# Kernel optimization log

Measured on AMD Instinct MI355X. Metric: run time of the kernel, lower is better.

The kernel has to match this reference:

```python
import jax, jax.numpy as jnp
import numpy as np

B, S, D = 2, 2048, 1024   # batch, seq, d_model
L, H = 256, 512           # d_latent, d_hidden (expert MLP)
E = 8                     # num_experts
SH = 512                  # shared-expert hidden (= d_hidden)


def setup_inputs() -> dict:
    key = jax.random.key(0)
    ks = jax.random.split(key, 12)
    s = 0.02
    return {
        "x": jax.random.normal(ks[0], (B, S, D), dtype=jnp.float32),
        "w_router": jax.random.normal(ks[1], (E, D), dtype=jnp.float32) * s,
        "w_down": jax.random.normal(ks[2], (L, D), dtype=jnp.float32) * s,
        "w_up": jax.random.normal(ks[3], (D, L), dtype=jnp.float32) * s,
        "w1_e": jax.random.normal(ks[4], (E, H, L), dtype=jnp.float32) * s,
        "wg_e": jax.random.normal(ks[5], (E, H, L), dtype=jnp.float32) * s,
        "w2_e": jax.random.normal(ks[6], (E, L, H), dtype=jnp.float32) * s,
        "w1_s": jax.random.normal(ks[7], (SH, D), dtype=jnp.float32) * s,
        "wg_s": jax.random.normal(ks[8], (SH, D), dtype=jnp.float32) * s,
        "w2_s": jax.random.normal(ks[9], (D, SH), dtype=jnp.float32) * s,
        "top_k": 2,
    }


def reference(x, w_router, w_down, w_up, w1_e, wg_e, w2_e, w1_s, wg_s, w2_s, top_k):
    Bq, Sq, Dq = x.shape
    T = Bq * Sq
    xf = x.reshape(T, Dq)

    # --- router (fp32 logits, softmax over top-k values) ---
    logits = xf.astype(jnp.float32) @ w_router.T            # (T, E)
    topk_val, topk_idx = jax.lax.top_k(logits, top_k)       # (T, k)
    topk_w = jax.nn.softmax(topk_val, axis=-1).astype(x.dtype)
    # dense combine weights (T, E); zero for unselected experts
    comb = jnp.zeros((T, E), dtype=x.dtype)
    comb = comb.at[jnp.arange(T)[:, None], topk_idx].add(topk_w)

    # --- shared latent down-projection ---
    lat = xf @ w_down.T                                     # (T, L)

    # --- all-expert SwiGLU in latent space, then weighted combine ---
    g = jax.nn.silu(jnp.einsum('tl,ehl->teh', lat, wg_e))   # (T, E, H)
    a = jnp.einsum('tl,ehl->teh', lat, w1_e)                # (T, E, H)
    ex = jnp.einsum('teh,elh->tel', g * a, w2_e)            # (T, E, L)
    routed_lat = jnp.einsum('te,tel->tl', comb, ex)         # (T, L)
    routed = routed_lat @ w_up.T                            # (T, D)

    # --- shared (dense) SwiGLU expert in d_model ---
    shared = (jax.nn.silu(xf @ wg_s.T) * (xf @ w1_s.T)) @ w2_s.T

    y = routed + shared
    return y.reshape(Bq, Sq, Dq)
```

## Files before the change

kernel.cpp:

```cpp
#include <hip/hip_runtime.h>
#include <hip/hip_bf16.h>
#include <math.h>

#define T_TOK 4096
#define D_MODEL 1024
#define L_LAT 256
#define H_HID 512
#define E_EXP 8
#define SH_HID 512
#define TOT_EROWS (2 * T_TOK)

typedef __bf16 bf16x8 __attribute__((ext_vector_type(8)));
typedef float f32x4 __attribute__((ext_vector_type(4)));

__device__ __forceinline__ unsigned short f2bf(float f) {
    union { float f; unsigned int u; } c{f};
    unsigned int r = (c.u + 0x7fffu + ((c.u >> 16) & 1u)) >> 16;
    return (unsigned short)r;
}
__device__ __forceinline__ float bf2f(unsigned short u) {
    union { unsigned int u; float f; } c{(unsigned int)u << 16};
    return c.f;
}

__device__ __forceinline__ void gload_lds16(const unsigned short* g, unsigned short* l) {
    __builtin_amdgcn_global_load_lds(
        (const __attribute__((address_space(1))) void*)g,
        (__attribute__((address_space(3))) void*)l,
        16, 0, 0);
}

__device__ __forceinline__ int swz64(int row, int s) {
    return s ^ (row & 7);
}

__global__ __launch_bounds__(256)
void cast_router_kernel(const float* __restrict__ x, const float* __restrict__ w_router,
                        const float* __restrict__ w_down, const float* __restrict__ wg_s,
                        const float* __restrict__ w1_s,
                        unsigned short* __restrict__ xb, unsigned short* __restrict__ wdb,
                        unsigned short* __restrict__ wgsb, unsigned short* __restrict__ w1sb,
                        int* __restrict__ topk_idx, float* __restrict__ topk_w)
{
    __shared__ float wlds[E_EXP * D_MODEL];
    int bid = blockIdx.x;
    int tid = threadIdx.x;

    if (bid < 4096) {
        int j = (bid * 256 + tid) * 4;
        float4 v = *(const float4*)(x + j);
        ushort4 o = { f2bf(v.x), f2bf(v.y), f2bf(v.z), f2bf(v.w) };
        *(ushort4*)(xb + j) = o;
        return;
    }
    if (bid >= 5120) {
        int i = (bid - 5120) * 256 + tid;
        const float* src; unsigned short* dst; int base;
        if      (i < 65536)  { src = w_down; dst = wdb;  base = 0; }
        else if (i < 196608) { src = wg_s;   dst = wgsb; base = 65536; }
        else                 { src = w1_s;   dst = w1sb; base = 196608; }
        int j = (i - base) * 4;
        float4 v = *(const float4*)(src + j);
        ushort4 o = { f2bf(v.x), f2bf(v.y), f2bf(v.z), f2bf(v.w) };
        *(ushort4*)(dst + j) = o;
        return;
    }

    int rb = bid - 4096;
    for (int i = tid * 4; i < E_EXP * D_MODEL; i += 256 * 4)
        *(float4*)(wlds + i) = *(const float4*)(w_router + i);
    __syncthreads();

    int wid = tid >> 6, lane = tid & 63;
    int t = rb * 4 + wid;
    const float* xr = x + (size_t)t * D_MODEL;
    float acc[E_EXP];
#pragma unroll
    for (int e = 0; e < E_EXP; ++e) acc[e] = 0.f;
#pragma unroll 4
    for (int i = 0; i < D_MODEL / 64; ++i) {
        int d = lane + i * 64;
        float xv = xr[d];
#pragma unroll
        for (int e = 0; e < E_EXP; ++e)
            acc[e] = fmaf(xv, wlds[e * D_MODEL + d], acc[e]);
    }
#pragma unroll
    for (int e = 0; e < E_EXP; ++e)
        for (int off = 32; off > 0; off >>= 1)
            acc[e] += __shfl_xor(acc[e], off, 64);
    if (lane == 0) {
        int i0 = 0; float v0 = acc[0];
#pragma unroll
        for (int e = 1; e < E_EXP; ++e) if (acc[e] > v0) { v0 = acc[e]; i0 = e; }
        int i1 = -1; float v1 = -INFINITY;
#pragma unroll
        for (int e = 0; e < E_EXP; ++e) if (e != i0 && acc[e] > v1) { v1 = acc[e]; i1 = e; }
        float e1 = expf(v1 - v0);
        topk_idx[2 * t] = i0; topk_idx[2 * t + 1] = i1;
        topk_w[2 * t] = 1.f / (1.f + e1);
        topk_w[2 * t + 1] = e1 / (1.f + e1);
    }
}

__device__ void bucket_body(const int* __restrict__ topk_idx,
                            int* __restrict__ counts, int* __restrict__ offsets,
                            int* __restrict__ tok_of_row, int* __restrict__ row_of_pair,
                            int* sb)
{
    int* s_wavecnt  = sb;
    int* s_wavebase = sb + 32;
    int* s_tot      = sb + 64;
    int* s_off      = sb + 72;
    int tid = threadIdx.x, wave = tid >> 6, lane = tid & 63;
    int base_i = tid * 32;

    int cnt[E_EXP];
#pragma unroll
    for (int e = 0; e < E_EXP; ++e) cnt[e] = 0;
#pragma unroll
    for (int j = 0; j < 32; ++j) {
        int e = topk_idx[base_i + j];
#pragma unroll
        for (int q = 0; q < E_EXP; ++q) cnt[q] += (e == q) ? 1 : 0;
    }
    int excl[E_EXP];
#pragma unroll
    for (int e = 0; e < E_EXP; ++e) {
        int v = cnt[e];
#pragma unroll
        for (int off = 1; off < 64; off <<= 1) {
            int u = __shfl_up(v, off, 64);
            v += (lane >= off) ? u : 0;
        }
        excl[e] = v - cnt[e];
        if (lane == 63) s_wavecnt[wave * 8 + e] = v;
    }
    __syncthreads();
    if (tid < E_EXP) {
        int tot = 0;
        for (int w = 0; w < 4; ++w) tot += s_wavecnt[w * 8 + tid];
        s_tot[tid] = tot;
        counts[tid] = tot;
    }
    __syncthreads();
    if (tid == 0) {
        int off = 0;
        for (int e = 0; e < E_EXP; ++e) { s_off[e] = off; offsets[e] = off; off += s_tot[e]; }
    }
    __syncthreads();
    if (tid < E_EXP) {
        int run = s_off[tid];
        for (int w = 0; w < 4; ++w) { s_wavebase[w * 8 + tid] = run; run += s_wavecnt[w * 8 + tid]; }
    }
    __syncthreads();
    int tb[E_EXP];
#pragma unroll
    for (int e = 0; e < E_EXP; ++e) tb[e] = s_wavebase[wave * 8 + e] + excl[e];
#pragma unroll
    for (int j = 0; j < 32; ++j) {
        int item = base_i + j;
        int e = topk_idx[item];
        int p = 0;
#pragma unroll
        for (int q = 0; q < E_EXP; ++q) if (e == q) { p = tb[q]; tb[q] = p + 1; }
        tok_of_row[p] = item >> 1;
        row_of_pair[item] = p;
    }
}

template<bool DUAL, bool SILU, bool EXPERT, bool GATHER, int OUT_MODE>
__device__ void gemm_tile(unsigned short* As, unsigned short* Bs0, unsigned short* Bs1,
                          int m0, int n0, int e,
                          const unsigned short* __restrict__ A,
                          const unsigned short* __restrict__ B0g,
                          const unsigned short* __restrict__ B1g,
                          void* __restrict__ Cv,
                          int M, int K, int ldc,
                          const int* __restrict__ tok_of_row,
                          const int* __restrict__ offsets,
                          const int* __restrict__ counts,
                          long strideB)
{
    int m_base = EXPERT ? offsets[e] : 0;
    int m_count = EXPERT ? counts[e] : M;
    if (m0 >= m_count) return;

    const unsigned short* B0 = B0g + (EXPERT ? (size_t)e * strideB : 0);
    const unsigned short* B1 = DUAL ? (B1g + (EXPERT ? (size_t)e * strideB : 0)) : nullptr;

    int tid = threadIdx.x;
    int r8 = tid >> 3, slot = tid & 7;

    const unsigned short* aptr[4];
#pragma unroll
    for (int r = 0; r < 4; ++r) {
        int rl = r * 32 + r8;
        int mrow = m0 + rl;
        if (mrow >= m_count) mrow = m_count - 1;
        long grow;
        if (GATHER)      grow = tok_of_row[m_base + mrow];
        else if (EXPERT) grow = m_base + mrow;
        else             grow = mrow;
        aptr[r] = A + (size_t)grow * K + swz64(rl, slot) * 8;
    }
    const unsigned short* bptr0[2];
    const unsigned short* bptr1[2];
#pragma unroll
    for (int r = 0; r < 2; ++r) {
        int rl = r * 32 + r8;
        int gs = swz64(rl, slot) * 8;
        bptr0[r] = B0 + (size_t)(n0 + rl) * K + gs;
        if (DUAL) bptr1[r] = B1 + (size_t)(n0 + rl) * K + gs;
    }
    unsigned short* As_dst  = As  + tid * 8;
    unsigned short* Bs0_dst = Bs0 + tid * 8;
    unsigned short* Bs1_dst = DUAL ? (Bs1 + tid * 8) : nullptr;

    int wave = tid >> 6, lane = tid & 63;
    int wm0 = (wave >> 1) * 64, wn0 = (wave & 1) * 32;
    int l15 = lane & 15, kg = lane >> 4;

    f32x4 acc0[4][2] = {};
    f32x4 acc1[DUAL ? 4 : 1][DUAL ? 2 : 1] = {};

    for (int k0 = 0; k0 < K; k0 += 64) {
#pragma unroll
        for (int r = 0; r < 4; ++r)
            gload_lds16(aptr[r] + k0, As_dst + r * 2048);
#pragma unroll
        for (int r = 0; r < 2; ++r) {
            gload_lds16(bptr0[r] + k0, Bs0_dst + r * 2048);
            if constexpr (DUAL) gload_lds16(bptr1[r] + k0, Bs1_dst + r * 2048);
        }
        __syncthreads();

        bf16x8 af[2][4];
#pragma unroll
        for (int kh = 0; kh < 2; ++kh)
#pragma unroll
            for (int mf = 0; mf < 4; ++mf) {
                int row = wm0 + mf * 16 + l15;
                af[kh][mf] = *reinterpret_cast<const bf16x8*>(As + row * 64 + swz64(row, kh * 4 + kg) * 8);
            }
        bf16x8 bf0[2][2], bf1[2][2];
#pragma unroll
        for (int kh = 0; kh < 2; ++kh)
#pragma unroll
            for (int nf = 0; nf < 2; ++nf) {
                int row = wn0 + nf * 16 + l15;
                bf0[kh][nf] = *reinterpret_cast<const bf16x8*>(Bs0 + row * 64 + swz64(row, kh * 4 + kg) * 8);
                if constexpr (DUAL)
                    bf1[kh][nf] = *reinterpret_cast<const bf16x8*>(Bs1 + row * 64 + swz64(row, kh * 4 + kg) * 8);
            }
#pragma unroll
        for (int kh = 0; kh < 2; ++kh)
#pragma unroll
            for (int mf = 0; mf < 4; ++mf)
#pragma unroll
                for (int nf = 0; nf < 2; ++nf) {
                    acc0[mf][nf] = __builtin_amdgcn_mfma_f32_16x16x32_bf16(af[kh][mf], bf0[kh][nf], acc0[mf][nf], 0, 0, 0);
                    if constexpr (DUAL)
                        acc1[mf][nf] = __builtin_amdgcn_mfma_f32_16x16x32_bf16(af[kh][mf], bf1[kh][nf], acc1[mf][nf], 0, 0, 0);
                }
        __syncthreads();
    }

#pragma unroll
    for (int mf = 0; mf < 4; ++mf) {
#pragma unroll
        for (int r4 = 0; r4 < 4; ++r4) {
            int mrow = m0 + wm0 + mf * 16 + kg * 4 + r4;
            if (mrow >= m_count) continue;
            size_t crow = (size_t)((EXPERT ? m_base : 0) + mrow) * ldc + n0 + wn0;
#pragma unroll
            for (int nf = 0; nf < 2; ++nf) {
                float v = acc0[mf][nf][r4];
                if constexpr (SILU) {
                    float g = v;
                    float a = acc1[mf][nf][r4];
                    v = (g / (1.f + expf(-g))) * a;
                }
                int col = nf * 16 + l15;
                if constexpr (OUT_MODE == 1)      ((unsigned short*)Cv)[crow + col] = f2bf(v);
                else if constexpr (OUT_MODE == 2) ((float*)Cv)[crow + col] += v;
                else                              ((float*)Cv)[crow + col] = v;
            }
        }
    }
}

__global__ __launch_bounds__(256)
void k_main(const unsigned short* __restrict__ x_bf,
            const unsigned short* __restrict__ wdown_bf,
            const unsigned short* __restrict__ wgs_bf,
            const unsigned short* __restrict__ w1s_bf,
            const float* __restrict__ wg_e, const float* __restrict__ w1_e,
            const float* __restrict__ w2_e,
            const float* __restrict__ w_up, const float* __restrict__ w2_s,
            unsigned short* __restrict__ lat_bf,
            unsigned short* __restrict__ hs,
            unsigned short* __restrict__ wge_bf, unsigned short* __restrict__ w1e_bf,
            unsigned short* __restrict__ w2e_bf, unsigned short* __restrict__ wup_bf,
            unsigned short* __restrict__ w2s_bf,
            const int* __restrict__ topk_idx,
            int* __restrict__ counts, int* __restrict__ offsets,
            int* __restrict__ tok_of_row, int* __restrict__ row_of_pair)
{
    __shared__ __align__(16) unsigned short As[128 * 64];
    __shared__ __align__(16) unsigned short Bs0[64 * 64];
    __shared__ __align__(16) unsigned short Bs1[64 * 64];

    int bid = blockIdx.x;
    int tid = threadIdx.x;

    if (bid == 384) {
        bucket_body(topk_idx, counts, offsets, tok_of_row, row_of_pair, (int*)As);
        return;
    }
    if (bid > 384) {
        int i = (bid - 385) * 256 + tid;
        const float* src; unsigned short* dst; int base;
        if      (i < 262144) { src = wg_e; dst = wge_bf; base = 0; }
        else if (i < 524288) { src = w1_e; dst = w1e_bf; base = 262144; }
        else if (i < 786432) { src = w2_e; dst = w2e_bf; base = 524288; }
        else if (i < 851968) { src = w_up; dst = wup_bf; base = 786432; }
        else                 { src = w2_s; dst = w2s_bf; base = 851968; }
        int j = (i - base) * 4;
        float4 v = *(const float4*)(src + j);
        ushort4 o = { f2bf(v.x), f2bf(v.y), f2bf(v.z), f2bf(v.w) };
        *(ushort4*)(dst + j) = o;
        return;
    }

    int xq = bid & 31, y = bid >> 5;
    if (y < 4) {
        gemm_tile<false, false, false, false, 1>(As, Bs0, Bs1, xq * 128, y * 64, 0,
            x_bf, wdown_bf, nullptr, lat_bf, T_TOK, D_MODEL, L_LAT,
            nullptr, nullptr, nullptr, 0);
    } else {
        gemm_tile<true, true, false, false, 1>(As, Bs0, Bs1, xq * 128, (y - 4) * 64, 0,
            x_bf, wgs_bf, w1s_bf, hs, T_TOK, D_MODEL, SH_HID,
            nullptr, nullptr, nullptr, 0);
    }
}

__global__ __launch_bounds__(256)
void k_exp_sh(const unsigned short* __restrict__ lat_bf,
              const unsigned short* __restrict__ wge_bf,
              const unsigned short* __restrict__ w1e_bf,
              const unsigned short* __restrict__ hs,
              const unsigned short* __restrict__ w2s_bf,
              unsigned short* __restrict__ hbuf_bf,
              float* __restrict__ out,
              const int* __restrict__ tok_of_row,
              const int* __restrict__ offsets,
              const int* __restrict__ counts)
{
    __shared__ __align__(16) unsigned short As[128 * 64];
    __shared__ __align__(16) unsigned short Bs0[64 * 64];
    __shared__ __align__(16) unsigned short Bs1[64 * 64];

    int bid = blockIdx.x;
    if (bid < 4096) {
        int xq = bid >> 6, e = (bid >> 3) & 7, y = bid & 7;
        gemm_tile<true, true, true, true, 1>(As, Bs0, Bs1, xq * 128, y * 64, e,
            lat_bf, wge_bf, w1e_bf, hbuf_bf, 0, L_LAT, H_HID,
            tok_of_row, offsets, counts, (long)H_HID * L_LAT);
    } else {
        int idx = bid - 4096;
        int xq = idx & 31, y = idx >> 5;
        gemm_tile<false, false, false, false, 0>(As, Bs0, Bs1, xq * 128, y * 64, 0,
            hs, w2s_bf, nullptr, out, T_TOK, SH_HID, D_MODEL,
            nullptr, nullptr, nullptr, 0);
    }
}

__global__ __launch_bounds__(256)
void k_expdown(const unsigned short* __restrict__ hbuf_bf,
               const unsigned short* __restrict__ w2e_bf,
               unsigned short* __restrict__ ex_bf,
               const int* __restrict__ offsets,
               const int* __restrict__ counts)
{
    __shared__ __align__(16) unsigned short As[128 * 64];
    __shared__ __align__(16) unsigned short Bs0[64 * 64];
    __shared__ __align__(16) unsigned short Bs1[8];
    gemm_tile<false, false, true, false, 1>(As, Bs0, Bs1,
        blockIdx.x * 128, blockIdx.y * 64, blockIdx.z,
        hbuf_bf, w2e_bf, nullptr, ex_bf, 0, H_HID, L_LAT,
        nullptr, offsets, counts, (long)L_LAT * H_HID);
}

__global__ void combine_kernel(const unsigned short* __restrict__ ex,
                               const int* __restrict__ row_of_pair,
                               const float* __restrict__ topk_w,
                               unsigned short* __restrict__ rlat)
{
    int i = blockIdx.x * 256 + threadIdx.x;
    int t = i >> 6;
    int l4 = (i & 63) * 4;
    int r0 = row_of_pair[2 * t], r1 = row_of_pair[2 * t + 1];
    float w0 = topk_w[2 * t], w1 = topk_w[2 * t + 1];
    ushort4 a = *(const ushort4*)(ex + (size_t)r0 * L_LAT + l4);
    ushort4 b = *(const ushort4*)(ex + (size_t)r1 * L_LAT + l4);
    ushort4 o = { f2bf(w0 * bf2f(a.x) + w1 * bf2f(b.x)),
                  f2bf(w0 * bf2f(a.y) + w1 * bf2f(b.y)),
                  f2bf(w0 * bf2f(a.z) + w1 * bf2f(b.z)),
                  f2bf(w0 * bf2f(a.w) + w1 * bf2f(b.w)) };
    *(ushort4*)(rlat + (size_t)t * L_LAT + l4) = o;
}

__global__ __launch_bounds__(256)
void k_final(const unsigned short* __restrict__ rlat,
             const unsigned short* __restrict__ wup_bf,
             float* __restrict__ out)
{
    __shared__ __align__(16) unsigned short As[128 * 64];
    __shared__ __align__(16) unsigned short Bs0[64 * 64];
    __shared__ __align__(16) unsigned short Bs1[8];
    gemm_tile<false, false, false, false, 2>(As, Bs0, Bs1,
        blockIdx.x * 128, blockIdx.y * 64, 0,
        rlat, wup_bf, nullptr, out, T_TOK, L_LAT, D_MODEL,
        nullptr, nullptr, nullptr, 0);
}

extern "C" void kernel_launch(void* const* d_in, const int* in_sizes, int n_in,
                              void* d_out, int out_size, void* d_ws, size_t ws_size,
                              hipStream_t stream)
{
    const float* x        = (const float*)d_in[0];
    const float* w_router = (const float*)d_in[1];
    const float* w_down   = (const float*)d_in[2];
    const float* w_up     = (const float*)d_in[3];
    const float* w1_e     = (const float*)d_in[4];
    const float* wg_e     = (const float*)d_in[5];
    const float* w2_e     = (const float*)d_in[6];
    const float* w1_s     = (const float*)d_in[7];
    const float* wg_s     = (const float*)d_in[8];
    const float* w2_s     = (const float*)d_in[9];
    float* out = (float*)d_out;

    char* ws = (char*)d_ws;
    size_t off = 0;
    auto alloc = [&](size_t bytes) -> void* {
        void* p = ws + off;
        off += (bytes + 255) & ~(size_t)255;
        return p;
    };
    unsigned short* x_bf    = (unsigned short*)alloc((size_t)T_TOK * D_MODEL * 2);
    unsigned short* lat_bf  = (unsigned short*)alloc((size_t)T_TOK * L_LAT * 2);
    unsigned short* hs      = (unsigned short*)alloc((size_t)T_TOK * SH_HID * 2);
    unsigned short* rlat    = (unsigned short*)alloc((size_t)T_TOK * L_LAT * 2);
    unsigned short* ex_bf   = (unsigned short*)alloc((size_t)TOT_EROWS * L_LAT * 2);
    unsigned short* wdown_bf= (unsigned short*)alloc((size_t)L_LAT * D_MODEL * 2);
    unsigned short* wge_bf  = (unsigned short*)alloc((size_t)E_EXP * H_HID * L_LAT * 2);
    unsigned short* w1e_bf  = (unsigned short*)alloc((size_t)E_EXP * H_HID * L_LAT * 2);
    unsigned short* w2e_bf  = (unsigned short*)alloc((size_t)E_EXP * L_LAT * H_HID * 2);
    unsigned short* wgs_bf  = (unsigned short*)alloc((size_t)SH_HID * D_MODEL * 2);
    unsigned short* w1s_bf  = (unsigned short*)alloc((size_t)SH_HID * D_MODEL * 2);
    unsigned short* wup_bf  = (unsigned short*)alloc((size_t)D_MODEL * L_LAT * 2);
    unsigned short* w2s_bf  = (unsigned short*)alloc((size_t)D_MODEL * SH_HID * 2);
    int*   topk_idx    = (int*)alloc(T_TOK * 2 * 4);
    float* topk_w      = (float*)alloc(T_TOK * 2 * 4);
    int*   tok_of_row  = (int*)alloc(T_TOK * 2 * 4);
    int*   row_of_pair = (int*)alloc(T_TOK * 2 * 4);
    int*   counts      = (int*)alloc(E_EXP * 4);
    int*   offsets     = (int*)alloc(E_EXP * 4);
    unsigned short* hbuf_bf = x_bf;

    cast_router_kernel<<<6400, 256, 0, stream>>>(
        x, w_router, w_down, wg_s, w1_s,
        x_bf, wdown_bf, wgs_bf, w1s_bf, topk_idx, topk_w);

    k_main<<<4225, 256, 0, stream>>>(
        x_bf, wdown_bf, wgs_bf, w1s_bf, wg_e, w1_e, w2_e, w_up, w2_s,
        lat_bf, hs, wge_bf, w1e_bf, w2e_bf, wup_bf, w2s_bf,
        topk_idx, counts, offsets, tok_of_row, row_of_pair);

    k_exp_sh<<<4608, 256, 0, stream>>>(
        lat_bf, wge_bf, w1e_bf, hs, w2s_bf, hbuf_bf, out,
        tok_of_row, offsets, counts);

    k_expdown<<<dim3(TOT_EROWS / 128, L_LAT / 64, E_EXP), 256, 0, stream>>>(
        hbuf_bf, w2e_bf, ex_bf, offsets, counts);

    combine_kernel<<<T_TOK * L_LAT / 4 / 256, 256, 0, stream>>>(
        ex_bf, row_of_pair, topk_w, rlat);

    k_final<<<dim3(T_TOK / 128, D_MODEL / 64), 256, 0, stream>>>(rlat, wup_bf, out);
}
```

Before: 91.10 us.

## Fuse top-k combine into up-projection GEMM and widen tiles to 128x128

Adds a 128x128-tile GEMM variant. It is used for the shared down-projection, the expert down-projection and the final up-projection. The final GEMM now gathers the two expert rows per token and blends them with the top-k weights while loading the A tile, so the separate combine kernel and its rlat buffer are no longer needed. The blend path uses plain vector loads rather than direct global-to-LDS loads, and the larger tiles halve the block counts, which could reduce occupancy or load balance.

```diff
diff --git a/kernel.cpp b/kernel.cpp
--- a/kernel.cpp
+++ b/kernel.cpp
@@ -281,6 +281,140 @@
                     float a = acc1[mf][nf][r4];
                     v = (g / (1.f + expf(-g))) * a;
                 }
+                int col = nf * 16 + l15;
+                if constexpr (OUT_MODE == 1) ((unsigned short*)Cv)[crow + col] = f2bf(v);
+                else                         ((float*)Cv)[crow + col] = v;
+            }
+        }
+    }
+}
+
+template<bool EXPERT, int OUT_MODE, bool BLEND>
+__device__ void gemm_tile_n128(unsigned short* SM,
+                               int m0, int n0, int e,
+                               const unsigned short* __restrict__ A,
+                               const unsigned short* __restrict__ B0g,
+                               void* __restrict__ Cv,
+                               int M, int K, int ldc,
+                               const int* __restrict__ offsets,
+                               const int* __restrict__ counts,
+                               long strideB,
+                               const int* __restrict__ row_of_pair,
+                               const float* __restrict__ topk_w)
+{
+    unsigned short* As = SM;
+    unsigned short* Bs = SM + 128 * 64;
+
+    int m_base = EXPERT ? offsets[e] : 0;
+    int m_count = EXPERT ? counts[e] : M;
+    if (m0 >= m_count) return;
+
+    const unsigned short* B0 = B0g + (EXPERT ? (size_t)e * strideB : 0);
+
+    int tid = threadIdx.x;
+    int r8 = tid >> 3, slot = tid & 7;
+
+    const unsigned short* aptr[4];
+    const unsigned short* a2ptr[4];
+    float wa[4], wb[4];
+#pragma unroll
+    for (int r = 0; r < 4; ++r) {
+        int rl = r * 32 + r8;
+        int mrow = m0 + rl;
+        if (mrow >= m_count) mrow = m_count - 1;
+        if constexpr (BLEND) {
+            int t = m0 + rl;
+            int rp0 = row_of_pair[2 * t], rp1 = row_of_pair[2 * t + 1];
+            wa[r] = topk_w[2 * t]; wb[r] = topk_w[2 * t + 1];
+            aptr[r]  = A + (size_t)rp0 * K + swz64(rl, slot) * 8;
+            a2ptr[r] = A + (size_t)rp1 * K + swz64(rl, slot) * 8;
+        } else {
+            long grow = EXPERT ? (long)(m_base + mrow) : (long)mrow;
+            aptr[r] = A + (size_t)grow * K + swz64(rl, slot) * 8;
+        }
+    }
+    const unsigned short* bptr[4];
+#pragma unroll
+    for (int r = 0; r < 4; ++r) {
+        int rl = r * 32 + r8;
+        bptr[r] = B0 + (size_t)(n0 + rl) * K + swz64(rl, slot) * 8;
+    }
+    unsigned short* As_dst = As + tid * 8;
+    unsigned short* Bs_dst = Bs + tid * 8;
+
+    int wave = tid >> 6, lane = tid & 63;
+    int wm0 = (wave >> 1) * 64, wn0 = (wave & 1) * 64;
+    int l15 = lane & 15, kg = lane >> 4;
+
+    f32x4 acc[4][4] = {};
+
+    for (int k0 = 0; k0 < K; k0 += 64) {
+        if constexpr (BLEND) {
+#pragma unroll
+            for (int r = 0; r < 4; ++r) {
+                ushort4 u0 = *(const ushort4*)(aptr[r] + k0);
+                ushort4 u1 = *(const ushort4*)(aptr[r] + k0 + 4);
+                ushort4 v0 = *(const ushort4*)(a2ptr[r] + k0);
+                ushort4 v1 = *(const ushort4*)(a2ptr[r] + k0 + 4);
+                ushort4 lo = { f2bf(wa[r] * bf2f(u0.x) + wb[r] * bf2f(v0.x)),
+                               f2bf(wa[r] * bf2f(u0.y) + wb[r] * bf2f(v0.y)),
+                               f2bf(wa[r] * bf2f(u0.z) + wb[r] * bf2f(v0.z)),
+                               f2bf(wa[r] * bf2f(u0.w) + wb[r] * bf2f(v0.w)) };
+                ushort4 hi = { f2bf(wa[r] * bf2f(u1.x) + wb[r] * bf2f(v1.x)),
+                               f2bf(wa[r] * bf2f(u1.y) + wb[r] * bf2f(v1.y)),
+                               f2bf(wa[r] * bf2f(u1.z) + wb[r] * bf2f(v1.z)),
+                               f2bf(wa[r] * bf2f(u1.w) + wb[r] * bf2f(v1.w)) };
+                *(ushort4*)(As_dst + r * 2048) = lo;
+                *(ushort4*)(As_dst + r * 2048 + 4) = hi;
+                ushort4 b0 = *(const ushort4*)(bptr[r] + k0);
+                ushort4 b1 = *(const ushort4*)(bptr[r] + k0 + 4);
+                *(ushort4*)(Bs_dst + r * 2048) = b0;
+                *(ushort4*)(Bs_dst + r * 2048 + 4) = b1;
+            }
+        } else {
+#pragma unroll
+            for (int r = 0; r < 4; ++r)
+                gload_lds16(aptr[r] + k0, As_dst + r * 2048);
+#pragma unroll
+            for (int r = 0; r < 4; ++r)
+                gload_lds16(bptr[r] + k0, Bs_dst + r * 2048);
+        }
+        __syncthreads();
+
+        bf16x8 af[2][4], bfr[2][4];
+#pragma unroll
+        for (int kh = 0; kh < 2; ++kh) {
+#pragma unroll
+            for (int mf = 0; mf < 4; ++mf) {
+                int row = wm0 + mf * 16 + l15;
+                af[kh][mf] = *reinterpret_cast<const bf16x8*>(As + row * 64 + swz64(row, kh * 4 + kg) * 8);
+            }
+#pragma unroll
+            for (int nf = 0; nf < 4; ++nf) {
+                int row = wn0 + nf * 16 + l15;
+                bfr[kh][nf] = *reinterpret_cast<const bf16x8*>(Bs + row * 64 + swz64(row, kh * 4 + kg) * 8);
+            }
+        }
+#pragma unroll
+        for (int kh = 0; kh < 2; ++kh)
+#pragma unroll
+            for (int mf = 0; mf < 4; ++mf)
+#pragma unroll
+                for (int nf = 0; nf < 4; ++nf)
+                    acc[mf][nf] = __builtin_amdgcn_mfma_f32_16x16x32_bf16(af[kh][mf], bfr[kh][nf], acc[mf][nf], 0, 0, 0);
+        __syncthreads();
+    }
+
+#pragma unroll
+    for (int mf = 0; mf < 4; ++mf) {
+#pragma unroll
+        for (int r4 = 0; r4 < 4; ++r4) {
+            int mrow = m0 + wm0 + mf * 16 + kg * 4 + r4;
+            if (mrow >= m_count) continue;
+            size_t crow = (size_t)((EXPERT ? m_base : 0) + mrow) * ldc + n0 + wn0;
+#pragma unroll
+            for (int nf = 0; nf < 4; ++nf) {
+                float v = acc[mf][nf][r4];
                 int col = nf * 16 + l15;
                 if constexpr (OUT_MODE == 1)      ((unsigned short*)Cv)[crow + col] = f2bf(v);
                 else if constexpr (OUT_MODE == 2) ((float*)Cv)[crow + col] += v;
@@ -307,15 +441,16 @@
             int* __restrict__ counts, int* __restrict__ offsets,
             int* __restrict__ tok_of_row, int* __restrict__ row_of_pair)
 {
-    __shared__ __align__(16) unsigned short As[128 * 64];
-    __shared__ __align__(16) unsigned short Bs0[64 * 64];
-    __shared__ __align__(16) unsigned short Bs1[64 * 64];
+    __shared__ __align__(16) unsigned short SM[16384];
+    unsigned short* As  = SM;
+    unsigned short* Bs0 = SM + 8192;
+    unsigned short* Bs1 = SM + 12288;
 
     int bid = blockIdx.x;
     int tid = threadIdx.x;
 
     if (bid == 384) {
-        bucket_body(topk_idx, counts, offsets, tok_of_row, row_of_pair, (int*)As);
+        bucket_body(topk_idx, counts, offsets, tok_of_row, row_of_pair, (int*)SM);
         return;
     }
     if (bid > 384) {
@@ -357,22 +492,20 @@
               const int* __restrict__ offsets,
               const int* __restrict__ counts)
 {
-    __shared__ __align__(16) unsigned short As[128 * 64];
-    __shared__ __align__(16) unsigned short Bs0[64 * 64];
-    __shared__ __align__(16) unsigned short Bs1[64 * 64];
-
+    __shared__ __align__(16) unsigned short SM[16384];
     int bid = blockIdx.x;
     if (bid < 4096) {
         int xq = bid >> 6, e = (bid >> 3) & 7, y = bid & 7;
-        gemm_tile<true, true, true, true, 1>(As, Bs0, Bs1, xq * 128, y * 64, e,
+        gemm_tile<true, true, true, true, 1>(SM, SM + 8192, SM + 12288,
+            xq * 128, y * 64, e,
             lat_bf, wge_bf, w1e_bf, hbuf_bf, 0, L_LAT, H_HID,
             tok_of_row, offsets, counts, (long)H_HID * L_LAT);
     } else {
         int idx = bid - 4096;
         int xq = idx & 31, y = idx >> 5;
-        gemm_tile<false, false, false, false, 0>(As, Bs0, Bs1, xq * 128, y * 64, 0,
-            hs, w2s_bf, nullptr, out, T_TOK, SH_HID, D_MODEL,
-            nullptr, nullptr, nullptr, 0);
+        gemm_tile_n128<false, 0, false>(SM, xq * 128, y * 128, 0,
+            hs, w2s_bf, out, T_TOK, SH_HID, D_MODEL,
+            nullptr, nullptr, 0, nullptr, nullptr);
     }
 }
 
@@ -383,46 +516,25 @@
                const int* __restrict__ offsets,
                const int* __restrict__ counts)
 {
-    __shared__ __align__(16) unsigned short As[128 * 64];
-    __shared__ __align__(16) unsigned short Bs0[64 * 64];
-    __shared__ __align__(16) unsigned short Bs1[8];
-    gemm_tile<false, false, true, false, 1>(As, Bs0, Bs1,
-        blockIdx.x * 128, blockIdx.y * 64, blockIdx.z,
-        hbuf_bf, w2e_bf, nullptr, ex_bf, 0, H_HID, L_LAT,
-        nullptr, offsets, counts, (long)L_LAT * H_HID);
-}
-
-__global__ void combine_kernel(const unsigned short* __restrict__ ex,
-                               const int* __restrict__ row_of_pair,
-                               const float* __restrict__ topk_w,
-                               unsigned short* __restrict__ rlat)
-{
-    int i = blockIdx.x * 256 + threadIdx.x;
-    int t = i >> 6;
-    int l4 = (i & 63) * 4;
-    int r0 = row_of_pair[2 * t], r1 = row_of_pair[2 * t + 1];
-    float w0 = topk_w[2 * t], w1 = topk_w[2 * t + 1];
-    ushort4 a = *(const ushort4*)(ex + (size_t)r0 * L_LAT + l4);
-    ushort4 b = *(const ushort4*)(ex + (size_t)r1 * L_LAT + l4);
-    ushort4 o = { f2bf(w0 * bf2f(a.x) + w1 * bf2f(b.x)),
-                  f2bf(w0 * bf2f(a.y) + w1 * bf2f(b.y)),
-                  f2bf(w0 * bf2f(a.z) + w1 * bf2f(b.z)),
-                  f2bf(w0 * bf2f(a.w) + w1 * bf2f(b.w)) };
-    *(ushort4*)(rlat + (size_t)t * L_LAT + l4) = o;
+    __shared__ __align__(16) unsigned short SM[16384];
+    gemm_tile_n128<true, 1, false>(SM,
+        blockIdx.x * 128, blockIdx.y * 128, blockIdx.z,
+        hbuf_bf, w2e_bf, ex_bf, 0, H_HID, L_LAT,
+        offsets, counts, (long)L_LAT * H_HID, nullptr, nullptr);
 }
 
 __global__ __launch_bounds__(256)
-void k_final(const unsigned short* __restrict__ rlat,
+void k_final(const unsigned short* __restrict__ ex_bf,
              const unsigned short* __restrict__ wup_bf,
+             const int* __restrict__ row_of_pair,
+             const float* __restrict__ topk_w,
              float* __restrict__ out)
 {
-    __shared__ __align__(16) unsigned short As[128 * 64];
-    __shared__ __align__(16) unsigned short Bs0[64 * 64];
-    __shared__ __align__(16) unsigned short Bs1[8];
-    gemm_tile<false, false, false, false, 2>(As, Bs0, Bs1,
-        blockIdx.x * 128, blockIdx.y * 64, 0,
-        rlat, wup_bf, nullptr, out, T_TOK, L_LAT, D_MODEL,
-        nullptr, nullptr, nullptr, 0);
+    __shared__ __align__(16) unsigned short SM[16384];
+    gemm_tile_n128<false, 2, true>(SM,
+        blockIdx.x * 128, blockIdx.y * 128, 0,
+        ex_bf, wup_bf, out, T_TOK, L_LAT, D_MODEL,
+        nullptr, nullptr, 0, row_of_pair, topk_w);
 }
 
 extern "C" void kernel_launch(void* const* d_in, const int* in_sizes, int n_in,
@@ -451,7 +563,6 @@
     unsigned short* x_bf    = (unsigned short*)alloc((size_t)T_TOK * D_MODEL * 2);
     unsigned short* lat_bf  = (unsigned short*)alloc((size_t)T_TOK * L_LAT * 2);
     unsigned short* hs      = (unsigned short*)alloc((size_t)T_TOK * SH_HID * 2);
-    unsigned short* rlat    = (unsigned short*)alloc((size_t)T_TOK * L_LAT * 2);
     unsigned short* ex_bf   = (unsigned short*)alloc((size_t)TOT_EROWS * L_LAT * 2);
     unsigned short* wdown_bf= (unsigned short*)alloc((size_t)L_LAT * D_MODEL * 2);
     unsigned short* wge_bf  = (unsigned short*)alloc((size_t)E_EXP * H_HID * L_LAT * 2);
@@ -478,15 +589,13 @@
         lat_bf, hs, wge_bf, w1e_bf, w2e_bf, wup_bf, w2s_bf,
         topk_idx, counts, offsets, tok_of_row, row_of_pair);
 
-    k_exp_sh<<<4608, 256, 0, stream>>>(
+    k_exp_sh<<<4352, 256, 0, stream>>>(
         lat_bf, wge_bf, w1e_bf, hs, w2s_bf, hbuf_bf, out,
         tok_of_row, offsets, counts);
 
-    k_expdown<<<dim3(TOT_EROWS / 128, L_LAT / 64, E_EXP), 256, 0, stream>>>(
+    k_expdown<<<dim3(TOT_EROWS / 128, L_LAT / 128, E_EXP), 256, 0, stream>>>(
         hbuf_bf, w2e_bf, ex_bf, offsets, counts);
 
-    combine_kernel<<<T_TOK * L_LAT / 4 / 256, 256, 0, stream>>>(
-        ex_bf, row_of_pair, topk_w, rlat);
-
-    k_final<<<dim3(T_TOK / 128, D_MODEL / 64), 256, 0, stream>>>(rlat, wup_bf, out);
-}
+    k_final<<<dim3(T_TOK / 128, D_MODEL / 128), 256, 0, stream>>>(
+        ex_bf, wup_bf, row_of_pair, topk_w, out);
+}
```

After: 91.27 us. No clear change (+0.2%).
